# Performance work log

Measured on AMD Instinct MI355X. Metric: run time of the kernel, lower is better.

The kernel has to match this reference:

```python
import jax, jax.numpy as jnp
import numpy as np

DIM = 1024
HEAD = 8
SPLIT = DIM // HEAD
EPS = 1e-6


def layernorm(x, gamma, beta):
    m = jnp.mean(x, axis=-1, keepdims=True)
    v = jnp.mean(jnp.square(x - m), axis=-1, keepdims=True)
    return (x - m) / jnp.sqrt(v + EPS) * gamma + beta


def setup_inputs() -> dict:
    key = jax.random.key(0)
    ks = jax.random.split(key, 6)
    s = 0.02
    return {
        "x": jax.random.normal(ks[0], (4, 2048, DIM), dtype=jnp.float32),
        "W_in": jax.random.normal(ks[1], (DIM, DIM), dtype=jnp.float32) * s,
        "gamma": jnp.ones((DIM,), jnp.float32),
        "beta": jnp.zeros((DIM,), jnp.float32),
        "Wq": jax.random.normal(ks[2], (HEAD, SPLIT, SPLIT), dtype=jnp.float32) * s,
        "Wk": jax.random.normal(ks[3], (HEAD, SPLIT, SPLIT), dtype=jnp.float32) * s,
        "Wv": jax.random.normal(ks[4], (HEAD, SPLIT, SPLIT), dtype=jnp.float32) * s,
        "Wf": jax.random.normal(ks[5], (DIM, DIM), dtype=jnp.float32) * s,
        "bf": jnp.zeros((DIM,), jnp.float32),
    }


def reference(x, W_in, gamma, beta, Wq, Wk, Wv, Wf, bf):
    B, S, _ = x.shape
    mod = x @ W_in  # [B,S,DIM], Dense no bias
    # pre-norm then split into heads: [B,S,HEAD,SPLIT]
    h = layernorm(mod, gamma, beta).reshape(B, S, HEAD, SPLIT)
    # per-head Q/K/V projections (batched over heads instead of Python loop)
    q = jnp.einsum('bshd,hde->bhse', h, Wq)
    k = jnp.einsum('bshd,hde->bhse', h, Wk)
    v = jnp.einsum('bshd,hde->bhse', h, Wv)
    # keras Attention(): unscaled dot-product scores (use_scale=False)
    scores = jnp.einsum('bhqe,bhke->bhqk', q, k)
    attn = jax.nn.softmax(scores, axis=-1)
    o = jnp.einsum('bhqk,bhke->bqhe', attn, v).reshape(B, S, DIM)
    mod = mod + o  # residual
    # FFN residual with shared LayerNorm params and ELU Dense
    mod = mod + jax.nn.elu(layernorm(mod, gamma, beta) @ Wf + bf)
    return mod
```

## Files before the change

### kernel.cpp

```cpp
#include <hip/hip_runtime.h>
#include <hip/hip_bf16.h>

#define DIMN 1024
#define NHEAD 8
#define ESPL 128
#define NB 4
#define SEQ 2048
#define NROWS (NB * SEQ)
#define LNEPS 1e-6f
#define L2E 1.442695041f

typedef unsigned short u16;
typedef unsigned int u32;
typedef __attribute__((ext_vector_type(8))) short short8;
typedef __attribute__((ext_vector_type(4))) short s16x4;
typedef __attribute__((ext_vector_type(4))) float f32x4;

__device__ __forceinline__ u16 f2bf(float f) {
  u32 u = __float_as_uint(f);
  u += 0x7FFFu + ((u >> 16) & 1u);
  return (u16)(u >> 16);
}

__device__ __forceinline__ u32 pk2bf(float a, float b) {
  u32 r;
  asm("v_cvt_pk_bf16_f32 %0, %1, %2" : "=v"(r) : "v"(a), "v"(b));
  return r;
}

__device__ __forceinline__ uint2 pack4bf(float4 v) {
  uint2 r;
  r.x = pk2bf(v.x, v.y);
  r.y = pk2bf(v.z, v.w);
  return r;
}

__device__ __forceinline__ float fexp2(float x) {
  float r;
  asm("v_exp_f32 %0, %1" : "=v"(r) : "v"(x));
  return r;
}

__device__ __forceinline__ float eluf(float x) { return x > 0.f ? x : expm1f(x); }

__device__ __forceinline__ void gl2lds16(const u16* g, u16* l) {
  __builtin_amdgcn_global_load_lds((const __attribute__((address_space(1))) u32*)g,
                                   (__attribute__((address_space(3))) u32*)l, 16, 0, 0);
}

__global__ __launch_bounds__(256) void ln_apply(const float* __restrict__ modp,
                                                const float* __restrict__ gamma,
                                                const float* __restrict__ beta,
                                                const float* __restrict__ s1p,
                                                const float* __restrict__ s2p,
                                                u16* __restrict__ outb) {
  int base = (blockIdx.x * 256 + threadIdx.x) * 4;
  int row = base >> 10, col = base & 1023;
  float s1 = s1p[row], s2 = s2p[row];
  float mu = s1 * (1.f / DIMN);
  float rsd = rsqrtf(fmaxf(s2 * (1.f / DIMN) - mu * mu, 0.f) + LNEPS);
  float4 v = *(const float4*)(modp + base);
  float4 g = *(const float4*)(gamma + col);
  float4 bb = *(const float4*)(beta + col);
  v.x = (v.x - mu) * rsd * g.x + bb.x;
  v.y = (v.y - mu) * rsd * g.y + bb.y;
  v.z = (v.z - mu) * rsd * g.z + bb.z;
  v.w = (v.w - mu) * rsd * g.w + bb.w;
  *(uint2*)(outb + base) = pack4bf(v);
}

__device__ __forceinline__ void wtrans_body(u16 (*tl)[68], const float* __restrict__ src,
                                            u16* __restrict__ dst, int K, int N, int n0,
                                            int k0) {
  const int t = threadIdx.x;
  const int r = t >> 2;
#pragma unroll
  for (int j = 0; j < 4; j++) {
    int f = (t & 3) + j * 4;
    float4 v = *(const float4*)(src + (size_t)(k0 + r) * N + n0 + f * 4);
    *(uint2*)&tl[r][f * 4] = pack4bf(v);
  }
  __syncthreads();
#pragma unroll
  for (int j = 0; j < 4; j++) {
    int f = (t & 3) + j * 4;
    ushort4 o;
    o.x = tl[f * 4 + 0][r];
    o.y = tl[f * 4 + 1][r];
    o.z = tl[f * 4 + 2][r];
    o.w = tl[f * 4 + 3][r];
    *(ushort4*)(dst + (size_t)(n0 + r) * K + k0 + f * 4) = o;
  }
}

__global__ __launch_bounds__(256) void prep_fused(
    const float* __restrict__ x, u16* __restrict__ xb, const float* __restrict__ W_in,
    u16* __restrict__ wt1, const float* __restrict__ Wf, u16* __restrict__ wt2,
    const float* __restrict__ Wq, const float* __restrict__ Wk, const float* __restrict__ Wv,
    u16* __restrict__ dq, u16* __restrict__ dk, u16* __restrict__ dv) {
  __shared__ u16 tl[64][68];
  const int bid = blockIdx.x;
  if (bid < NROWS) {
    int base = (bid * 256 + threadIdx.x) * 4;
    *(uint2*)(xb + base) = pack4bf(*(const float4*)(x + base));
  } else if (bid < NROWS + 512) {
    int z = bid - NROWS;
    const float* s = (z & 256) ? Wf : W_in;
    u16* d = (z & 256) ? wt2 : wt1;
    z &= 255;
    wtrans_body(tl, s, d, DIMN, DIMN, (z & 15) * 64, (z >> 4) * 64);
  } else {
    int z = bid - NROWS - 512;
    int xy = z & 3, zz = z >> 2;
    int mi = zz >> 3, hh = zz & 7;
    const float* s = (mi == 0) ? Wq : (mi == 1) ? Wk : Wv;
    u16* d = (mi == 0) ? dq : (mi == 1) ? dk : dv;
    s += (size_t)hh * ESPL * ESPL;
    d += (size_t)hh * ESPL * ESPL;
    wtrans_body(tl, s, d, ESPL, ESPL, (xy & 1) * 64, (xy >> 1) * 64);
  }
}

template <int MODE>
__global__ __launch_bounds__(256, 2) void gemm_bf16(
    const u16* __restrict__ A, const u16* __restrict__ Bt, const float* __restrict__ resid,
    const float* __restrict__ bias, float* __restrict__ s1p, float* __restrict__ s2p,
    float* __restrict__ C) {
  __shared__ __align__(16) char lds[65536];
  const int t = threadIdx.x;
  const int w = t >> 6, lane = t & 63, quad = lane >> 4, l16 = lane & 15;
  const int wm = w & 1, wn = w >> 1;
  const int lin = blockIdx.x + gridDim.x * blockIdx.y;
  const int xcd = lin & 7, slot = lin >> 3;
  const int m0 = (xcd * 8 + (slot >> 3)) * 128;
  const int n0 = (slot & 7) * 128;

  auto stage = [&](int koff, int bi) {
    const u16* ag = A + (size_t)m0 * DIMN + koff;
    const u16* bg = Bt + (size_t)n0 * DIMN + koff;
    u16* As = (u16*)(lds + bi * 32768);
    u16* Bs = (u16*)(lds + bi * 32768 + 16384);
#pragma unroll
    for (int i = 0; i < 4; i++) {
      int pbase = (w * 4 + i) * 64;
      int p = pbase + lane;
      int r = p >> 3, c8 = (p & 7) ^ (r & 7);
      gl2lds16(ag + (size_t)r * DIMN + c8 * 8, As + pbase * 8);
      gl2lds16(bg + (size_t)r * DIMN + c8 * 8, Bs + pbase * 8);
    }
  };

  f32x4 acc[4][4];
#pragma unroll
  for (int mt = 0; mt < 4; mt++)
#pragma unroll
    for (int nt = 0; nt < 4; nt++) acc[mt][nt] = (f32x4){0.f, 0.f, 0.f, 0.f};

  stage(0, 0);
  __syncthreads();
  for (int kt = 0; kt < DIMN / 64; kt++) {
    if (kt + 1 < DIMN / 64) stage((kt + 1) * 64, (kt + 1) & 1);
    const u16* As = (const u16*)(lds + (kt & 1) * 32768);
    const u16* Bs = (const u16*)(lds + (kt & 1) * 32768 + 16384);
#pragma unroll
    for (int ks = 0; ks < 2; ks++) {
      short8 af[4], bfr[4];
#pragma unroll
      for (int mt = 0; mt < 4; mt++) {
        int row = wm * 64 + mt * 16 + l16;
        int pc = (ks * 4 + quad) ^ (row & 7);
        af[mt] = *(const short8*)(As + row * 64 + pc * 8);
      }
#pragma unroll
      for (int nt = 0; nt < 4; nt++) {
        int row = wn * 64 + nt * 16 + l16;
        int pc = (ks * 4 + quad) ^ (row & 7);
        bfr[nt] = *(const short8*)(Bs + row * 64 + pc * 8);
      }
#pragma unroll
      for (int mt = 0; mt < 4; mt++)
#pragma unroll
        for (int nt = 0; nt < 4; nt++)
          acc[mt][nt] = __builtin_amdgcn_mfma_f32_16x16x32_bf16(bfr[nt], af[mt], acc[mt][nt], 0, 0, 0);
    }
    __syncthreads();
  }
#pragma unroll
  for (int mt = 0; mt < 4; mt++) {
    int row = m0 + wm * 64 + mt * 16 + l16;
    float s1 = 0.f, s2 = 0.f;
#pragma unroll
    for (int nt = 0; nt < 4; nt++) {
      int col = n0 + wn * 64 + nt * 16 + quad * 4;
      size_t off = (size_t)row * DIMN + col;
      f32x4 v = acc[mt][nt];
      if (MODE == 0) {
        *(f32x4*)(C + off) = v;
        s1 += (v[0] + v[1]) + (v[2] + v[3]);
        s2 += (v[0] * v[0] + v[1] * v[1]) + (v[2] * v[2] + v[3] * v[3]);
      } else {
        float4 rv = *(const float4*)(resid + off);
        float4 bv = *(const float4*)(bias + col);
        float4 o;
        o.x = rv.x + eluf(v[0] + bv.x);
        o.y = rv.y + eluf(v[1] + bv.y);
        o.z = rv.z + eluf(v[2] + bv.z);
        o.w = rv.w + eluf(v[3] + bv.w);
        *(float4*)(C + off) = o;
      }
    }
    if (MODE == 0) {
      s1 += __shfl_xor(s1, 16);
      s1 += __shfl_xor(s1, 32);
      s2 += __shfl_xor(s2, 16);
      s2 += __shfl_xor(s2, 32);
      if (quad == 0) {
        atomicAdd(s1p + row, s1);
        atomicAdd(s2p + row, s2);
      }
    }
  }
}

#define QP 136

__global__ __launch_bounds__(256) void qkv_mfma(
    const float* __restrict__ modp, const u16* __restrict__ wqt, const u16* __restrict__ wkt,
    const u16* __restrict__ wvt, const float* __restrict__ gamma, const float* __restrict__ beta,
    const float* __restrict__ s1p, const float* __restrict__ s2p, u16* __restrict__ qo,
    u16* __restrict__ ko, u16* __restrict__ vto) {
  __shared__ u16 Asl[128 * QP];
  __shared__ u16 Bsl[128 * QP];
  const int t = threadIdx.x;
  const int w = t >> 6, lane = t & 63, quad = lane >> 4, l16 = lane & 15;
  const int wm = w & 1, wn = w >> 1;
  const int lin = blockIdx.x + gridDim.x * blockIdx.y;
  const int xcd = lin & 7, slot = lin >> 3;
  const int s0 = (slot >> 2) * 128;
  const int bh = (slot & 3) * 8 + xcd;
  const int b = bh >> 3, hh = bh & 7;
  const int sr8 = t >> 3, sf8 = t & 7;
#pragma unroll
  for (int p = 0; p < 4; p++) {
    int r = sr8 + 32 * p;
    int rowg = b * SEQ + s0 + r;
    float s1 = s1p[rowg], s2 = s2p[rowg];
    float mu = s1 * (1.f / DIMN);
    float rsd = rsqrtf(fmaxf(s2 * (1.f / DIMN) - mu * mu, 0.f) + LNEPS);
    const float* ap = modp + (size_t)rowg * DIMN + hh * ESPL;
#pragma unroll
    for (int j = 0; j < 4; j++) {
      int f = sf8 + j * 8;
      float4 v = *(const float4*)(ap + f * 4);
      float4 g = *(const float4*)(gamma + hh * ESPL + f * 4);
      float4 bb = *(const float4*)(beta + hh * ESPL + f * 4);
      v.x = (v.x - mu) * rsd * g.x + bb.x;
      v.y = (v.y - mu) * rsd * g.y + bb.y;
      v.z = (v.z - mu) * rsd * g.z + bb.z;
      v.w = (v.w - mu) * rsd * g.w + bb.w;
      *(uint2*)(Asl + r * QP + f * 4) = pack4bf(v);
    }
  }
  __syncthreads();
  short8 afr[4][4];
#pragma unroll
  for (int k4 = 0; k4 < 4; k4++)
#pragma unroll
    for (int mt = 0; mt < 4; mt++)
      afr[k4][mt] = *(const short8*)(Asl + (wm * 64 + mt * 16 + l16) * QP + k4 * 32 + quad * 8);

  const u16* Ws[3] = {wqt, wkt, wvt};
  for (int mi = 0; mi < 3; mi++) {
    __syncthreads();
    const u16* wsrc = Ws[mi] + ((size_t)hh << 14);
#pragma unroll
    for (int p = 0; p < 4; p++) {
      int r = sr8 + 32 * p;
#pragma unroll
      for (int j = 0; j < 2; j++) {
        int f = sf8 + j * 8;
        *(uint4*)(Bsl + r * QP + f * 8) = *(const uint4*)(wsrc + r * ESPL + f * 8);
      }
    }
    __syncthreads();
    f32x4 acc[4][4];
#pragma unroll
    for (int mt = 0; mt < 4; mt++)
#pragma unroll
      for (int nt = 0; nt < 4; nt++) acc[mt][nt] = (f32x4){0.f, 0.f, 0.f, 0.f};
#pragma unroll
    for (int k4 = 0; k4 < 4; k4++) {
      short8 bfr[4];
#pragma unroll
      for (int nt = 0; nt < 4; nt++)
        bfr[nt] = *(const short8*)(Bsl + (wn * 64 + nt * 16 + l16) * QP + k4 * 32 + quad * 8);
      if (mi < 2) {
#pragma unroll
        for (int mt = 0; mt < 4; mt++)
#pragma unroll
          for (int nt = 0; nt < 4; nt++)
            acc[mt][nt] = __builtin_amdgcn_mfma_f32_16x16x32_bf16(bfr[nt], afr[k4][mt], acc[mt][nt], 0, 0, 0);
      } else {
#pragma unroll
        for (int mt = 0; mt < 4; mt++)
#pragma unroll
          for (int nt = 0; nt < 4; nt++)
            acc[mt][nt] = __builtin_amdgcn_mfma_f32_16x16x32_bf16(afr[k4][mt], bfr[nt], acc[mt][nt], 0, 0, 0);
      }
    }
    if (mi < 2) {
      u16* o = (mi == 0) ? qo : ko;
#pragma unroll
      for (int mt = 0; mt < 4; mt++) {
        int s = s0 + wm * 64 + mt * 16 + l16;
#pragma unroll
        for (int nt = 0; nt < 4; nt++) {
          int e0 = wn * 64 + nt * 16 + quad * 4;
          uint2 pk;
          pk.x = pk2bf(acc[mt][nt][0], acc[mt][nt][1]);
          pk.y = pk2bf(acc[mt][nt][2], acc[mt][nt][3]);
          *(uint2*)(o + ((size_t)bh * SEQ + s) * ESPL + e0) = pk;
        }
      }
    } else {
#pragma unroll
      for (int mt = 0; mt < 4; mt++)
#pragma unroll
        for (int nt = 0; nt < 4; nt++) {
          int e = wn * 64 + nt * 16 + l16;
          int sbase = s0 + wm * 64 + mt * 16 + quad * 4;
          uint2 pk;
          pk.x = pk2bf(acc[mt][nt][0], acc[mt][nt][1]);
          pk.y = pk2bf(acc[mt][nt][2], acc[mt][nt][3]);
          *(uint2*)(vto + ((size_t)bh * ESPL + e) * SEQ + sbase) = pk;
        }
    }
  }
}

#define RESCALE_THR 8.f

__global__ __launch_bounds__(512, 2) void attn_mfma(const u16* __restrict__ q,
                                                    const u16* __restrict__ kk,
                                                    const u16* __restrict__ vt,
                                                    float* __restrict__ modp,
                                                    float* __restrict__ s1p,
                                                    float* __restrict__ s2p) {
  __shared__ __align__(16) char lds[98304];
  const int t = threadIdx.x;
  const int w = t >> 6, lane = t & 63, quad = lane >> 4, l16 = lane & 15;
  const int lin = blockIdx.x + gridDim.x * blockIdx.y;
  const int xcd = lin & 7, slot = lin >> 3;
  const int qt = slot & 7;
  const int bh = xcd * 4 + (slot >> 3);
  const int b = bh >> 3, hh = bh & 7;
  const size_t qkbase = (size_t)bh * SEQ * ESPL;
  const int qrow0 = qt * 256 + w * 32;
  const u16* kg0 = kk + qkbase;
  const u16* vg0 = vt + qkbase;
  char* Pt = lds + 65536 + w * 4096;
  const int swz = (l16 & 7) << 4;

  short8 qf[2][4];
#pragma unroll
  for (int g = 0; g < 2; g++) {
    const u16* qrow = q + qkbase + (size_t)(qrow0 + g * 16 + l16) * ESPL + quad * 8;
#pragma unroll
    for (int kc = 0; kc < 4; kc++) qf[g][kc] = *(const short8*)(qrow + kc * 32);
  }

  float m_st[2] = {-1e30f, -1e30f}, l_st[2] = {0.f, 0.f};
  f32x4 oacc[2][8];
#pragma unroll
  for (int g = 0; g < 2; g++)
#pragma unroll
    for (int et = 0; et < 8; et++) oacc[g][et] = (f32x4){0.f, 0.f, 0.f, 0.f};

  auto stage = [&](int kt, int bi) {
    const u16* kg = kg0 + (size_t)kt * 64 * ESPL;
    const u16* vg = vg0 + (size_t)kt * 64;
    u16* Ksb = (u16*)(lds + bi * 32768);
    u16* Vsb = (u16*)(lds + bi * 32768 + 16384);
#pragma unroll
    for (int i = 0; i < 2; i++) {
      int pbase = w * 128 + i * 64;
      int p = pbase + lane;
      int r = p >> 4, c8 = (p & 15) ^ (r & 15);
      gl2lds16(kg + r * ESPL + c8 * 8, Ksb + pbase * 8);
      int e = p >> 3, v8 = (p & 7) ^ (e & 7);
      gl2lds16(vg + (size_t)e * SEQ + v8 * 8, Vsb + pbase * 8);
    }
  };

  stage(0, 0);
  __syncthreads();

  for (int kt = 0; kt < SEQ / 64; kt++) {
    if (kt + 1 < SEQ / 64) stage(kt + 1, (kt + 1) & 1);
    const u16* Ks = (const u16*)(lds + (kt & 1) * 32768);
    const u16* Vs = (const u16*)(lds + (kt & 1) * 32768 + 16384);
    f32x4 sacc[4][2];
#pragma unroll
    for (int mt = 0; mt < 4; mt++)
#pragma unroll
      for (int g = 0; g < 2; g++) sacc[mt][g] = (f32x4){0.f, 0.f, 0.f, 0.f};
    __builtin_amdgcn_s_setprio(1);
#pragma unroll
    for (int mt = 0; mt < 4; mt++) {
#pragma unroll
      for (int kc = 0; kc < 4; kc++) {
        short8 kf = *(const short8*)(Ks + (mt * 16 + l16) * 128 + (((kc * 4 + quad) ^ l16) << 3));
        sacc[mt][0] = __builtin_amdgcn_mfma_f32_16x16x32_bf16(kf, qf[0][kc], sacc[mt][0], 0, 0, 0);
        sacc[mt][1] = __builtin_amdgcn_mfma_f32_16x16x32_bf16(kf, qf[1][kc], sacc[mt][1], 0, 0, 0);
      }
    }
    __builtin_amdgcn_s_setprio(0);
    float alpha[2];
    bool updf[2];
#pragma unroll
    for (int g = 0; g < 2; g++) {
      const f32x4 a = sacc[0][g], b2 = sacc[1][g], c2 = sacc[2][g], d2 = sacc[3][g];
      float t0 = fmaxf(fmaxf(a[0], a[1]), a[2]);
      float t1 = fmaxf(fmaxf(a[3], b2[0]), b2[1]);
      float t2 = fmaxf(fmaxf(b2[2], b2[3]), c2[0]);
      float t3 = fmaxf(fmaxf(c2[1], c2[2]), c2[3]);
      float t4 = fmaxf(fmaxf(d2[0], d2[1]), d2[2]);
      float mloc = fmaxf(fmaxf(fmaxf(t0, t1), t2), fmaxf(fmaxf(t3, t4), d2[3]));
      mloc = fmaxf(mloc, __shfl_xor(mloc, 16));
      mloc = fmaxf(mloc, __shfl_xor(mloc, 32));
      updf[g] = !__all(mloc - m_st[g] <= RESCALE_THR);
      if (updf[g]) {
        float mnew = fmaxf(m_st[g], mloc);
        alpha[g] = fexp2((m_st[g] - mnew) * L2E);
        m_st[g] = mnew;
      } else {
        alpha[g] = 1.f;
      }
      const float mkn = -m_st[g] * L2E;
      float sum = 0.f;
#pragma unroll
      for (int mt = 0; mt < 4; mt++) {
        float p0 = fexp2(fmaf(sacc[mt][g][0], L2E, mkn));
        float p1 = fexp2(fmaf(sacc[mt][g][1], L2E, mkn));
        float p2 = fexp2(fmaf(sacc[mt][g][2], L2E, mkn));
        float p3 = fexp2(fmaf(sacc[mt][g][3], L2E, mkn));
        sum += (p0 + p1) + (p2 + p3);
        uint2 pkv = make_uint2(pk2bf(p0, p1), pk2bf(p2, p3));
        *(uint2*)(Pt + g * 2048 + l16 * 128 + ((mt * 32 + quad * 8) ^ swz)) = pkv;
      }
      sum += __shfl_xor(sum, 16);
      sum += __shfl_xor(sum, 32);
      l_st[g] = l_st[g] * alpha[g] + sum;
    }
    if (updf[0]) {
#pragma unroll
      for (int et = 0; et < 8; et++)
#pragma unroll
        for (int r = 0; r < 4; r++) oacc[0][et][r] *= alpha[0];
    }
    if (updf[1]) {
#pragma unroll
      for (int et = 0; et < 8; et++)
#pragma unroll
        for (int r = 0; r < 4; r++) oacc[1][et][r] *= alpha[1];
    }
    short8 pb[2][2];
#pragma unroll
    for (int g = 0; g < 2; g++)
#pragma unroll
      for (int mtp = 0; mtp < 2; mtp++)
        pb[g][mtp] = *(const short8*)(Pt + g * 2048 + l16 * 128 + ((mtp * 64 + quad * 16) ^ swz));
    __builtin_amdgcn_s_setprio(1);
#pragma unroll
    for (int et = 0; et < 8; et++) {
#pragma unroll
      for (int mtp = 0; mtp < 2; mtp++) {
        short8 vf8 = *(const short8*)(Vs + (size_t)(et * 16 + l16) * 64 +
                                      (((mtp * 4 + quad) ^ (l16 & 7)) << 3));
        oacc[0][et] = __builtin_amdgcn_mfma_f32_16x16x32_bf16(vf8, pb[0][mtp], oacc[0][et], 0, 0, 0);
        oacc[1][et] = __builtin_amdgcn_mfma_f32_16x16x32_bf16(vf8, pb[1][mtp], oacc[1][et], 0, 0, 0);
      }
    }
    __builtin_amdgcn_s_setprio(0);
    __syncthreads();
  }

#pragma unroll
  for (int g = 0; g < 2; g++) {
    float linv = 1.f / l_st[g];
    int qglob = qrow0 + g * 16 + l16;
    float* mp = modp + ((size_t)(b * SEQ + qglob)) * DIMN + hh * ESPL;
    float s1 = 0.f, s2 = 0.f;
#pragma unroll
    for (int et = 0; et < 8; et++) {
      int e0 = et * 16 + quad * 4;
      f32x4 ov = oacc[g][et];
      float4 mv = *(const float4*)(mp + e0);
      mv.x += ov[0] * linv;
      mv.y += ov[1] * linv;
      mv.z += ov[2] * linv;
      mv.w += ov[3] * linv;
      *(float4*)(mp + e0) = mv;
      s1 += (mv.x + mv.y) + (mv.z + mv.w);
      s2 += (mv.x * mv.x + mv.y * mv.y) + (mv.z * mv.z + mv.w * mv.w);
    }
    s1 += __shfl_xor(s1, 16);
    s1 += __shfl_xor(s1, 32);
    s2 += __shfl_xor(s2, 16);
    s2 += __shfl_xor(s2, 32);
    if (quad == 0) {
      atomicAdd(s1p + b * SEQ + qglob, s1);
      atomicAdd(s2p + b * SEQ + qglob, s2);
    }
  }
}

extern "C" void kernel_launch(void* const* d_in, const int* in_sizes, int n_in, void* d_out,
                              int out_size, void* d_ws, size_t ws_size, hipStream_t stream) {
  (void)in_sizes;
  (void)n_in;
  (void)out_size;
  (void)ws_size;
  const float* x = (const float*)d_in[0];
  const float* W_in = (const float*)d_in[1];
  const float* gamma = (const float*)d_in[2];
  const float* beta = (const float*)d_in[3];
  const float* Wq = (const float*)d_in[4];
  const float* Wk = (const float*)d_in[5];
  const float* Wv = (const float*)d_in[6];
  const float* Wf = (const float*)d_in[7];
  const float* bf = (const float*)d_in[8];
  float* out = (float*)d_out;

  char* ws = (char*)d_ws;
  const size_t MB = 1024ull * 1024;
  float* mod = (float*)ws;
  u16* qb = (u16*)(ws + 32 * MB);
  u16* kb = (u16*)(ws + 48 * MB);
  u16* vtb = (u16*)(ws + 64 * MB);
  float* sums = (float*)(ws + 80 * MB);
  float* s1a = sums;
  float* s2a = s1a + NROWS;
  float* s1b = s2a + NROWS;
  float* s2b = s1b + NROWS;
  u16* wqt = (u16*)(ws + 80 * MB + 4 * NROWS * sizeof(float));
  u16* wkt = wqt + NHEAD * ESPL * ESPL;
  u16* wvt = wkt + NHEAD * ESPL * ESPL;
  u16* wt2 = wvt + NHEAD * ESPL * ESPL;
  u16* wt1 = qb;
  u16* xb = kb;
  u16* modb = qb;

  hipMemsetAsync(sums, 0, 4 * NROWS * sizeof(float), stream);
  prep_fused<<<NROWS + 512 + 96, 256, 0, stream>>>(x, xb, W_in, wt1, Wf, wt2, Wq, Wk, Wv, wqt,
                                                   wkt, wvt);

  dim3 gg(DIMN / 128, NROWS / 128);
  gemm_bf16<0><<<gg, 256, 0, stream>>>(xb, wt1, nullptr, nullptr, s1a, s2a, mod);
  qkv_mfma<<<dim3(SEQ / 128, NB * NHEAD), 256, 0, stream>>>(mod, wqt, wkt, wvt, gamma, beta,
                                                            s1a, s2a, qb, kb, vtb);
  attn_mfma<<<dim3(SEQ / 256, NB * NHEAD), 512, 0, stream>>>(qb, kb, vtb, mod, s1b, s2b);
  ln_apply<<<NROWS * DIMN / 1024, 256, 0, stream>>>(mod, gamma, beta, s1b, s2b, modb);
  gemm_bf16<1><<<gg, 256, 0, stream>>>(modb, wt2, mod, bf, nullptr, nullptr, out);
}
```

Baseline: 284.9 us.

## Fuse second LayerNorm into FFN GEMM A-tile load; DMA QKV weights into LDS

After: 270.0 us. -5.2%, faster.

```diff
diff --git a/kernel.cpp b/kernel.cpp
--- a/kernel.cpp
+++ b/kernel.cpp
@@ -46,27 +46,6 @@
 __device__ __forceinline__ void gl2lds16(const u16* g, u16* l) {
   __builtin_amdgcn_global_load_lds((const __attribute__((address_space(1))) u32*)g,
                                    (__attribute__((address_space(3))) u32*)l, 16, 0, 0);
-}
-
-__global__ __launch_bounds__(256) void ln_apply(const float* __restrict__ modp,
-                                                const float* __restrict__ gamma,
-                                                const float* __restrict__ beta,
-                                                const float* __restrict__ s1p,
-                                                const float* __restrict__ s2p,
-                                                u16* __restrict__ outb) {
-  int base = (blockIdx.x * 256 + threadIdx.x) * 4;
-  int row = base >> 10, col = base & 1023;
-  float s1 = s1p[row], s2 = s2p[row];
-  float mu = s1 * (1.f / DIMN);
-  float rsd = rsqrtf(fmaxf(s2 * (1.f / DIMN) - mu * mu, 0.f) + LNEPS);
-  float4 v = *(const float4*)(modp + base);
-  float4 g = *(const float4*)(gamma + col);
-  float4 bb = *(const float4*)(beta + col);
-  v.x = (v.x - mu) * rsd * g.x + bb.x;
-  v.y = (v.y - mu) * rsd * g.y + bb.y;
-  v.z = (v.z - mu) * rsd * g.z + bb.z;
-  v.w = (v.w - mu) * rsd * g.w + bb.w;
-  *(uint2*)(outb + base) = pack4bf(v);
 }
 
 __device__ __forceinline__ void wtrans_body(u16 (*tl)[68], const float* __restrict__ src,
@@ -123,9 +102,10 @@
 
 template <int MODE>
 __global__ __launch_bounds__(256, 2) void gemm_bf16(
-    const u16* __restrict__ A, const u16* __restrict__ Bt, const float* __restrict__ resid,
-    const float* __restrict__ bias, float* __restrict__ s1p, float* __restrict__ s2p,
-    float* __restrict__ C) {
+    const u16* __restrict__ A, const u16* __restrict__ Bt, const float* __restrict__ Af,
+    const float* __restrict__ resid, const float* __restrict__ bias,
+    const float* __restrict__ gamma, const float* __restrict__ beta,
+    float* __restrict__ s1p, float* __restrict__ s2p, float* __restrict__ C) {
   __shared__ __align__(16) char lds[65536];
   const int t = threadIdx.x;
   const int w = t >> 6, lane = t & 63, quad = lane >> 4, l16 = lane & 15;
@@ -135,31 +115,103 @@
   const int m0 = (xcd * 8 + (slot >> 3)) * 128;
   const int n0 = (slot & 7) * 128;
 
-  auto stage = [&](int koff, int bi) {
+  auto stageB = [&](int koff, int bi) {
+    const u16* bg = Bt + (size_t)n0 * DIMN + koff;
+    u16* Bs = (u16*)(lds + bi * 32768 + 16384);
+#pragma unroll
+    for (int i = 0; i < 4; i++) {
+      int pbase = (w * 4 + i) * 64;
+      int p = pbase + lane;
+      int r = p >> 3, c8 = (p & 7) ^ (r & 7);
+      gl2lds16(bg + (size_t)r * DIMN + c8 * 8, Bs + pbase * 8);
+    }
+  };
+  auto stageA_dma = [&](int koff, int bi) {
     const u16* ag = A + (size_t)m0 * DIMN + koff;
-    const u16* bg = Bt + (size_t)n0 * DIMN + koff;
     u16* As = (u16*)(lds + bi * 32768);
-    u16* Bs = (u16*)(lds + bi * 32768 + 16384);
 #pragma unroll
     for (int i = 0; i < 4; i++) {
       int pbase = (w * 4 + i) * 64;
       int p = pbase + lane;
       int r = p >> 3, c8 = (p & 7) ^ (r & 7);
       gl2lds16(ag + (size_t)r * DIMN + c8 * 8, As + pbase * 8);
-      gl2lds16(bg + (size_t)r * DIMN + c8 * 8, Bs + pbase * 8);
     }
   };
 
+  float4 av0[4], av1[4];
+  float mu4[4], rs4[4];
+  if (MODE == 1) {
+#pragma unroll
+    for (int i = 0; i < 4; i++) {
+      int r = (t >> 3) + 32 * i;
+      float s1 = s1p[m0 + r], s2 = s2p[m0 + r];
+      float mu = s1 * (1.f / DIMN);
+      mu4[i] = mu;
+      rs4[i] = rsqrtf(fmaxf(s2 * (1.f / DIMN) - mu * mu, 0.f) + LNEPS);
+    }
+  }
+  auto ldA = [&](int koff) {
+#pragma unroll
+    for (int i = 0; i < 4; i++) {
+      int p = t + i * 256;
+      int r = p >> 3, c8 = (p & 7) ^ (r & 7);
+      const float* src = Af + (size_t)(m0 + r) * DIMN + koff + c8 * 8;
+      av0[i] = *(const float4*)(src);
+      av1[i] = *(const float4*)(src + 4);
+    }
+  };
+  auto wrA = [&](int koff, int bi) {
+    u16* As = (u16*)(lds + bi * 32768);
+#pragma unroll
+    for (int i = 0; i < 4; i++) {
+      int p = t + i * 256;
+      int r = p >> 3, c8 = (p & 7) ^ (r & 7);
+      int col = koff + c8 * 8;
+      float4 g0 = *(const float4*)(gamma + col);
+      float4 g1 = *(const float4*)(gamma + col + 4);
+      float4 b0 = *(const float4*)(beta + col);
+      float4 b1 = *(const float4*)(beta + col + 4);
+      float4 v0 = av0[i], v1 = av1[i];
+      v0.x = (v0.x - mu4[i]) * rs4[i] * g0.x + b0.x;
+      v0.y = (v0.y - mu4[i]) * rs4[i] * g0.y + b0.y;
+      v0.z = (v0.z - mu4[i]) * rs4[i] * g0.z + b0.z;
+      v0.w = (v0.w - mu4[i]) * rs4[i] * g0.w + b0.w;
+      v1.x = (v1.x - mu4[i]) * rs4[i] * g1.x + b1.x;
+      v1.y = (v1.y - mu4[i]) * rs4[i] * g1.y + b1.y;
+      v1.z = (v1.z - mu4[i]) * rs4[i] * g1.z + b1.z;
+      v1.w = (v1.w - mu4[i]) * rs4[i] * g1.w + b1.w;
+      uint4 pk;
+      pk.x = pk2bf(v0.x, v0.y);
+      pk.y = pk2bf(v0.z, v0.w);
+      pk.z = pk2bf(v1.x, v1.y);
+      pk.w = pk2bf(v1.z, v1.w);
+      *(uint4*)(As + (size_t)p * 8) = pk;
+    }
+  };
+
   f32x4 acc[4][4];
 #pragma unroll
   for (int mt = 0; mt < 4; mt++)
 #pragma unroll
     for (int nt = 0; nt < 4; nt++) acc[mt][nt] = (f32x4){0.f, 0.f, 0.f, 0.f};
 
-  stage(0, 0);
+  if (MODE == 1) {
+    ldA(0);
+    stageB(0, 0);
+    wrA(0, 0);
+  } else {
+    stageA_dma(0, 0);
+    stageB(0, 0);
+  }
   __syncthreads();
   for (int kt = 0; kt < DIMN / 64; kt++) {
-    if (kt + 1 < DIMN / 64) stage((kt + 1) * 64, (kt + 1) & 1);
+    if (kt + 1 < DIMN / 64) {
+      if (MODE == 1)
+        ldA((kt + 1) * 64);
+      else
+        stageA_dma((kt + 1) * 64, (kt + 1) & 1);
+      stageB((kt + 1) * 64, (kt + 1) & 1);
+    }
     const u16* As = (const u16*)(lds + (kt & 1) * 32768);
     const u16* Bs = (const u16*)(lds + (kt & 1) * 32768 + 16384);
 #pragma unroll
@@ -183,6 +235,7 @@
         for (int nt = 0; nt < 4; nt++)
           acc[mt][nt] = __builtin_amdgcn_mfma_f32_16x16x32_bf16(bfr[nt], af[mt], acc[mt][nt], 0, 0, 0);
     }
+    if (MODE == 1 && kt + 1 < DIMN / 64) wrA((kt + 1) * 64, (kt + 1) & 1);
     __syncthreads();
   }
 #pragma unroll
@@ -230,7 +283,7 @@
     const float* __restrict__ s1p, const float* __restrict__ s2p, u16* __restrict__ qo,
     u16* __restrict__ ko, u16* __restrict__ vto) {
   __shared__ u16 Asl[128 * QP];
-  __shared__ u16 Bsl[128 * QP];
+  __shared__ __align__(16) u16 Bsl[128 * 128];
   const int t = threadIdx.x;
   const int w = t >> 6, lane = t & 63, quad = lane >> 4, l16 = lane & 15;
   const int wm = w & 1, wn = w >> 1;
@@ -274,13 +327,11 @@
     __syncthreads();
     const u16* wsrc = Ws[mi] + ((size_t)hh << 14);
 #pragma unroll
-    for (int p = 0; p < 4; p++) {
-      int r = sr8 + 32 * p;
-#pragma unroll
-      for (int j = 0; j < 2; j++) {
-        int f = sf8 + j * 8;
-        *(uint4*)(Bsl + r * QP + f * 8) = *(const uint4*)(wsrc + r * ESPL + f * 8);
-      }
+    for (int i = 0; i < 8; i++) {
+      int pbase = w * 64 + i * 256;
+      int p = pbase + lane;
+      int r = p >> 4, c8 = (p & 15) ^ (r & 15);
+      gl2lds16(wsrc + r * ESPL + c8 * 8, Bsl + pbase * 8);
     }
     __syncthreads();
     f32x4 acc[4][4];
@@ -292,8 +343,10 @@
     for (int k4 = 0; k4 < 4; k4++) {
       short8 bfr[4];
 #pragma unroll
-      for (int nt = 0; nt < 4; nt++)
-        bfr[nt] = *(const short8*)(Bsl + (wn * 64 + nt * 16 + l16) * QP + k4 * 32 + quad * 8);
+      for (int nt = 0; nt < 4; nt++) {
+        int row = wn * 64 + nt * 16 + l16;
+        bfr[nt] = *(const short8*)(Bsl + row * 128 + (((k4 * 4 + quad) ^ l16) << 3));
+      }
       if (mi < 2) {
 #pragma unroll
         for (int mt = 0; mt < 4; mt++)
@@ -549,17 +602,16 @@
   u16* wt2 = wvt + NHEAD * ESPL * ESPL;
   u16* wt1 = qb;
   u16* xb = kb;
-  u16* modb = qb;
 
   hipMemsetAsync(sums, 0, 4 * NROWS * sizeof(float), stream);
   prep_fused<<<NROWS + 512 + 96, 256, 0, stream>>>(x, xb, W_in, wt1, Wf, wt2, Wq, Wk, Wv, wqt,
                                                    wkt, wvt);
 
   dim3 gg(DIMN / 128, NROWS / 128);
-  gemm_bf16<0><<<gg, 256, 0, stream>>>(xb, wt1, nullptr, nullptr, s1a, s2a, mod);
+  gemm_bf16<0><<<gg, 256, 0, stream>>>(xb, wt1, nullptr, nullptr, nullptr, nullptr, nullptr,
+                                       s1a, s2a, mod);
   qkv_mfma<<<dim3(SEQ / 128, NB * NHEAD), 256, 0, stream>>>(mod, wqt, wkt, wvt, gamma, beta,
                                                             s1a, s2a, qb, kb, vtb);
   attn_mfma<<<dim3(SEQ / 256, NB * NHEAD), 512, 0, stream>>>(qb, kb, vtb, mod, s1b, s2b);
-  ln_apply<<<NROWS * DIMN / 1024, 256, 0, stream>>>(mod, gamma, beta, s1b, s2b, modb);
-  gemm_bf16<1><<<gg, 256, 0, stream>>>(modb, wt2, mod, bf, nullptr, nullptr, out);
-}
+  gemm_bf16<1><<<gg, 256, 0, stream>>>(nullptr, wt2, mod, mod, bf, gamma, beta, s1b, s2b, out);
+}
```
